# Kernel optimization log

Measured on AMD Instinct MI355X. Metric: run time of the kernel, lower is better.

Reference implementation:

```python
import jax, jax.numpy as jnp
import numpy as np

H = 8      # n_heads
DK = 64    # d_k per head
EPS = 1e-5       # InstanceNorm1d eps
SLOPE = 0.01     # LeakyReLU negative slope


def setup_inputs() -> dict:
    key = jax.random.key(0)
    ks = jax.random.split(key, 6)
    B, C, L = 16, 256, 1024
    HD = H * DK  # 512
    return {
        "x": jax.random.normal(ks[0], (B, C, L), dtype=jnp.float32),
        "Wq": jax.random.normal(ks[1], (HD, C), dtype=jnp.float32) * 0.02,
        "Wk": jax.random.normal(ks[2], (HD, C), dtype=jnp.float32) * 0.02,
        "Wv": jax.random.normal(ks[3], (HD, C), dtype=jnp.float32) * 0.02,
        "Wo": jax.random.normal(ks[4], (C, HD), dtype=jnp.float32) * 0.02,
        "gamma": jax.random.normal(ks[5], (1,), dtype=jnp.float32),
    }


def reference(x, Wq, Wk, Wv, Wo, gamma):
    B, C, L = x.shape
    # conv1x1 projections (bias=False) == channel matmuls -> [B, H*DK, L]
    # then reshape/permute into heads: [B, H, L, DK]
    def proj(W):
        y = jnp.einsum('oc,bcl->bol', W, x)          # [B, H*DK, L]
        return y.reshape(B, H, DK, L).transpose(0, 1, 3, 2)  # [B, H, L, DK]

    q, k, v = proj(Wq), proj(Wk), proj(Wv)
    # softmax-free linear attention: (Q K^T / d_k) V
    logits = jnp.einsum('bhld,bhmd->bhlm', q, k) / DK  # [B, H, L, L]
    out = jnp.einsum('bhlm,bhmd->bhld', logits, v)     # [B, H, L, DK]
    # merge heads back to channel-first [B, H*DK, L]
    merged = out.transpose(0, 1, 3, 2).reshape(B, H * DK, L)
    # output conv1x1 -> [B, C, L]
    o = jnp.einsum('oc,bcl->bol', Wo, merged)
    # InstanceNorm1d (affine=False): normalize over L per (b, c)
    mu = jnp.mean(o, axis=-1, keepdims=True)
    var = jnp.var(o, axis=-1, keepdims=True)
    o = (o - mu) * jax.lax.rsqrt(var + EPS)
    # gamma-scaled residual + LeakyReLU
    y = o * gamma + x
    return jnp.where(y >= 0, y, SLOPE * y)
```

## Files before the change

kernel.cpp:

```cpp
#include <hip/hip_runtime.h>

typedef __bf16 bf16;
typedef bf16 bf16x8 __attribute__((ext_vector_type(8)));
typedef bf16 bf16x4 __attribute__((ext_vector_type(4)));
typedef float f32x4 __attribute__((ext_vector_type(4)));

#define EPS 1e-5f
#define SLOPE 0.01f

__device__ __forceinline__ void gld_lds16(const bf16* g, bf16* l) {
    __builtin_amdgcn_global_load_lds(
        (const __attribute__((address_space(1))) unsigned int*)g,
        (__attribute__((address_space(3))) unsigned int*)l, 16, 0, 0);
}

template<int LOG2T>
__device__ __forceinline__ void xcd_decode(int raw, int& b, int& t) {
    const int p = raw & 7, m = raw >> 3;
    b = ((m >> LOG2T) << 3) + p;
    t = m & ((1 << LOG2T) - 1);
}

__global__ __launch_bounds__(256) void prep_kernel(
    const float* __restrict__ x,
    const float* __restrict__ Wq, const float* __restrict__ Wk,
    const float* __restrict__ Wv, const float* __restrict__ Wo,
    bf16* __restrict__ xT, bf16* __restrict__ xB,
    bf16* __restrict__ WkB, bf16* __restrict__ WvB,
    bf16* __restrict__ WoB, bf16* __restrict__ WqT)
{
    __shared__ float tile[64][65];
    const int raw = blockIdx.x;
    int id;
    if (raw < 1024) {
        int b, t64; xcd_decode<6>(raw, b, t64);
        id = (b << 6) | t64;
    } else id = raw;
    const int t = threadIdx.x;
    if (id < 1024) {
        const int lt = id & 15, ct = (id >> 4) & 3, b = id >> 6;
        {
            const int cl = t >> 2;
            const int l4 = (t & 3) << 4;
            const float* src = x + (size_t)(b * 256 + ct * 64 + cl) * 1024 + lt * 64 + l4;
            float4 v0 = ((const float4*)src)[0];
            float4 v1 = ((const float4*)src)[1];
            float4 v2 = ((const float4*)src)[2];
            float4 v3 = ((const float4*)src)[3];
            bf16x8 r0, r1;
            r0[0]=(bf16)v0.x; r0[1]=(bf16)v0.y; r0[2]=(bf16)v0.z; r0[3]=(bf16)v0.w;
            r0[4]=(bf16)v1.x; r0[5]=(bf16)v1.y; r0[6]=(bf16)v1.z; r0[7]=(bf16)v1.w;
            r1[0]=(bf16)v2.x; r1[1]=(bf16)v2.y; r1[2]=(bf16)v2.z; r1[3]=(bf16)v2.w;
            r1[4]=(bf16)v3.x; r1[5]=(bf16)v3.y; r1[6]=(bf16)v3.z; r1[7]=(bf16)v3.w;
            bf16* xbd = xB + (size_t)(b * 256 + ct * 64 + cl) * 1024 + lt * 64 + l4;
            *(bf16x8*)xbd = r0;
            *(bf16x8*)(xbd + 8) = r1;
            float* tr = &tile[cl][l4];
            tr[0]=v0.x; tr[1]=v0.y; tr[2]=v0.z; tr[3]=v0.w;
            tr[4]=v1.x; tr[5]=v1.y; tr[6]=v1.z; tr[7]=v1.w;
            tr[8]=v2.x; tr[9]=v2.y; tr[10]=v2.z; tr[11]=v2.w;
            tr[12]=v3.x; tr[13]=v3.y; tr[14]=v3.z; tr[15]=v3.w;
        }
        __syncthreads();
        {
            const int lw = t >> 2;
            const int ec = (t & 3) << 4;
            bf16x8 o0, o1;
            #pragma unroll
            for (int ii = 0; ii < 8; ++ii) {
                o0[ii] = (bf16)tile[ec + ii][lw];
                o1[ii] = (bf16)tile[ec + 8 + ii][lw];
            }
            bf16* dst = xT + (size_t)(b * 1024 + lt * 64 + lw) * 256 + ct * 64 + ec;
            *(bf16x8*)dst = o0;
            *(bf16x8*)(dst + 8) = o1;
        }
    } else if (id < 1408) {
        const int i = (id - 1024) * 1024 + t * 4;
        const float* src; bf16* dst;
        if (i < 131072)      { src = Wk + i;            dst = WkB + i; }
        else if (i < 262144) { src = Wv + (i - 131072); dst = WvB + (i - 131072); }
        else                 { src = Wo + (i - 262144); dst = WoB + (i - 262144); }
        float4 v = *(const float4*)src;
        bf16x4 o;
        o[0]=(bf16)v.x; o[1]=(bf16)v.y; o[2]=(bf16)v.z; o[3]=(bf16)v.w;
        *(bf16x4*)dst = o;
    } else {
        const int id2 = id - 1408;
        const int h = id2 >> 2, ct = id2 & 3;
        {
            const int e  = t >> 2;
            const int c4 = (t & 3) << 4;
            const float* src = Wq + (size_t)(h * 64 + e) * 256 + ct * 64 + c4;
            float4 v0 = ((const float4*)src)[0];
            float4 v1 = ((const float4*)src)[1];
            float4 v2 = ((const float4*)src)[2];
            float4 v3 = ((const float4*)src)[3];
            float* tr = &tile[e][c4];
            tr[0]=v0.x; tr[1]=v0.y; tr[2]=v0.z; tr[3]=v0.w;
            tr[4]=v1.x; tr[5]=v1.y; tr[6]=v1.z; tr[7]=v1.w;
            tr[8]=v2.x; tr[9]=v2.y; tr[10]=v2.z; tr[11]=v2.w;
            tr[12]=v3.x; tr[13]=v3.y; tr[14]=v3.z; tr[15]=v3.w;
        }
        __syncthreads();
        {
            const int c  = t >> 2;
            const int e4 = (t & 3) << 4;
            bf16x8 o0, o1;
            #pragma unroll
            for (int ii = 0; ii < 8; ++ii) {
                o0[ii] = (bf16)tile[e4 + ii][c];
                o1[ii] = (bf16)tile[e4 + 8 + ii][c];
            }
            bf16* dst = WqT + (size_t)h * 16384 + (size_t)(ct * 64 + c) * 64 + e4;
            *(bf16x8*)dst = o0;
            *(bf16x8*)(dst + 8) = o1;
        }
    }
}

template<int KDIM, typename OutT>
__global__ __launch_bounds__(256) void gemm128_bt(
    const bf16* __restrict__ A, const bf16* __restrict__ Bt, OutT* __restrict__ C,
    long long sA, long long sBt, long long sC, int ldC)
{
    constexpr int NT = KDIM / 32;
    constexpr int NB = 5;
    __shared__ bf16 As[NB][128 * 32];
    __shared__ bf16 Bs[NB][128 * 32];
    int z, tt; xcd_decode<4>(blockIdx.x, z, tt);
    A  += (size_t)z * sA;
    Bt += (size_t)z * sBt;
    C  += (size_t)z * sC;
    const int m0 = (tt >> 3) * 128;
    const int n0 = (tt & 7) * 128;
    const int t = threadIdx.x, w = t >> 6, l = t & 63;
    const int srow = w * 16 + (l >> 2);
    const int ske  = (l & 3) * 8;
    const bf16* ga = A  + (size_t)(m0 + srow) * KDIM + ske;
    const bf16* gb = Bt + (size_t)(n0 + srow) * KDIM + ske;
    const int loff = srow * 32 + ske;
    const int lm = l & 15, lq = l >> 4;
    const int wm = (w & 1) * 64, wn = (w >> 1) * 64;

    #pragma unroll
    for (int i = 0; i < NB - 1; ++i) {
        const int k0 = i * 32;
        gld_lds16(ga + k0, &As[i][0] + loff);
        gld_lds16(ga + k0 + (size_t)64 * KDIM, &As[i][0] + 64 * 32 + loff);
        gld_lds16(gb + k0, &Bs[i][0] + loff);
        gld_lds16(gb + k0 + (size_t)64 * KDIM, &Bs[i][0] + 64 * 32 + loff);
    }

    f32x4 acc[4][4] = {};
    #pragma unroll
    for (int kt = 0; kt < NT; ++kt) {
        const int cur = kt % NB;
        const int stg = (kt + NB - 1) % NB;
        const int remain = NT - 1 - kt;
        if (remain >= 3)      asm volatile("s_waitcnt vmcnt(12)" ::: "memory");
        else if (remain == 2) asm volatile("s_waitcnt vmcnt(8)"  ::: "memory");
        else if (remain == 1) asm volatile("s_waitcnt vmcnt(4)"  ::: "memory");
        else                  asm volatile("s_waitcnt vmcnt(0)"  ::: "memory");
        __builtin_amdgcn_s_barrier();
        __builtin_amdgcn_sched_barrier(0);
        if (kt + NB - 1 < NT) {
            const int k0 = (kt + NB - 1) * 32;
            gld_lds16(ga + k0, &As[stg][0] + loff);
            gld_lds16(ga + k0 + (size_t)64 * KDIM, &As[stg][0] + 64 * 32 + loff);
            gld_lds16(gb + k0, &Bs[stg][0] + loff);
            gld_lds16(gb + k0 + (size_t)64 * KDIM, &Bs[stg][0] + 64 * 32 + loff);
        }
        bf16x8 af[4], bfr[4];
        #pragma unroll
        for (int i = 0; i < 4; ++i)
            af[i] = *(const bf16x8*)(&As[cur][0] + (wm + i * 16 + lm) * 32 + lq * 8);
        #pragma unroll
        for (int j = 0; j < 4; ++j)
            bfr[j] = *(const bf16x8*)(&Bs[cur][0] + (wn + j * 16 + lm) * 32 + lq * 8);
        #pragma unroll
        for (int i = 0; i < 4; ++i)
            #pragma unroll
            for (int j = 0; j < 4; ++j)
                acc[i][j] = __builtin_amdgcn_mfma_f32_16x16x32_bf16(af[i], bfr[j], acc[i][j], 0, 0, 0);
    }
    #pragma unroll
    for (int i = 0; i < 4; ++i)
        #pragma unroll
        for (int j = 0; j < 4; ++j) {
            const int row = m0 + wm + i * 16 + lq * 4;
            const int col = n0 + wn + j * 16 + lm;
            OutT* cp = C + (size_t)row * ldC + col;
            #pragma unroll
            for (int r = 0; r < 4; ++r)
                cp[(size_t)r * ldC] = (OutT)acc[i][j][r];
        }
}

template<int KDIM, typename OutT>
__global__ __launch_bounds__(256) void gemm64_bt(
    const bf16* __restrict__ A, const bf16* __restrict__ Bt, OutT* __restrict__ C,
    long long sA, long long sBt, long long sC, int ldC)
{
    constexpr int NT = KDIM / 32;
    constexpr int NB = 5;
    __shared__ bf16 As[NB][64 * 32];
    __shared__ bf16 Bs[NB][64 * 32];
    int z, tt; xcd_decode<4>(blockIdx.x, z, tt);
    A  += (size_t)z * sA;
    Bt += (size_t)z * sBt;
    C  += (size_t)z * sC;
    const int m0 = (tt & 3) * 64;
    const int n0 = (tt >> 2) * 64;
    const int t = threadIdx.x, w = t >> 6, l = t & 63;
    const int srow = t >> 2;
    const int ske  = (t & 3) * 8;
    const bf16* ga = A  + (size_t)(m0 + srow) * KDIM + ske;
    const bf16* gb = Bt + (size_t)(n0 + srow) * KDIM + ske;
    const int loff = srow * 32 + ske;
    const int lm = l & 15, lq = l >> 4;

    #pragma unroll
    for (int i = 0; i < NB - 1; ++i) {
        const int k0 = i * 32;
        gld_lds16(ga + k0, &As[i][0] + loff);
        gld_lds16(gb + k0, &Bs[i][0] + loff);
    }

    f32x4 acc[4] = {};
    #pragma unroll
    for (int kt = 0; kt < NT; ++kt) {
        const int cur = kt % NB;
        const int stg = (kt + NB - 1) % NB;
        const int remain = NT - 1 - kt;
        if (remain >= 3)      asm volatile("s_waitcnt vmcnt(6)" ::: "memory");
        else if (remain == 2) asm volatile("s_waitcnt vmcnt(4)" ::: "memory");
        else if (remain == 1) asm volatile("s_waitcnt vmcnt(2)" ::: "memory");
        else                  asm volatile("s_waitcnt vmcnt(0)" ::: "memory");
        __builtin_amdgcn_s_barrier();
        __builtin_amdgcn_sched_barrier(0);
        if (kt + NB - 1 < NT) {
            const int k0 = (kt + NB - 1) * 32;
            gld_lds16(ga + k0, &As[stg][0] + loff);
            gld_lds16(gb + k0, &Bs[stg][0] + loff);
        }
        bf16x8 af = *(const bf16x8*)(&As[cur][0] + (w * 16 + lm) * 32 + lq * 8);
        bf16x8 bfr[4];
        #pragma unroll
        for (int j = 0; j < 4; ++j)
            bfr[j] = *(const bf16x8*)(&Bs[cur][0] + (j * 16 + lm) * 32 + lq * 8);
        #pragma unroll
        for (int j = 0; j < 4; ++j)
            acc[j] = __builtin_amdgcn_mfma_f32_16x16x32_bf16(af, bfr[j], acc[j], 0, 0, 0);
    }
    #pragma unroll
    for (int j = 0; j < 4; ++j) {
        const int row = m0 + w * 16 + lq * 4;
        const int col = n0 + j * 16 + lm;
        OutT* cp = C + (size_t)row * ldC + col;
        #pragma unroll
        for (int r = 0; r < 4; ++r)
            cp[(size_t)r * ldC] = (OutT)acc[j][r];
    }
}

struct __align__(16) Tm2Ph1 { bf16 P[16384]; bf16 Va[16384]; bf16 Gr[4][8192]; };
struct __align__(16) Tm2Ph2 { bf16 P[16384]; bf16 Kc[16384]; bf16 Qb[16384]; bf16 Tb[4096]; };
union  __align__(16) Tm2Sm  { Tm2Ph1 p1; Tm2Ph2 p2; };

__global__ __launch_bounds__(256) void tm2_kernel(
    const bf16* __restrict__ G, const bf16* __restrict__ WvB,
    const bf16* __restrict__ WkB, const bf16* __restrict__ WqT,
    bf16* __restrict__ WmT)
{
    __shared__ Tm2Sm sm;
    int b, h; xcd_decode<3>(blockIdx.x, b, h);
    const bf16* Gg = G   + (size_t)b * 65536;
    const bf16* Vg = WvB + (size_t)h * 16384;
    const bf16* Kg = WkB + (size_t)h * 16384;
    const bf16* Qg = WqT + (size_t)h * 16384;
    const int t = threadIdx.x, w = t >> 6, l = t & 63;
    const int lm = l & 15, lq = l >> 4;

    #pragma unroll
    for (int it = 0; it < 4; ++it) {
        const int idx = it * 256 + t;
        const int r = idx >> 2, s2 = idx & 3;
        gld_lds16(Gg + (size_t)r * 256 + 0 * 32 + (s2 ^ (r & 3)) * 8,
                  &sm.p1.Gr[0][0] + r * 32 + s2 * 8);
    }
    #pragma unroll
    for (int it = 0; it < 8; ++it) {
        const int idx = it * 256 + t;
        const int r = idx >> 5, s = idx & 31;
        gld_lds16(Vg + (size_t)r * 256 + (s ^ (r & 7)) * 8,
                  sm.p1.Va + r * 256 + s * 8);
    }
    #pragma unroll
    for (int tb = 1; tb < 3; ++tb) {
        #pragma unroll
        for (int it = 0; it < 4; ++it) {
            const int idx = it * 256 + t;
            const int r = idx >> 2, s2 = idx & 3;
            gld_lds16(Gg + (size_t)r * 256 + tb * 32 + (s2 ^ (r & 3)) * 8,
                      &sm.p1.Gr[tb][0] + r * 32 + s2 * 8);
        }
    }

    f32x4 accP[4][4] = {};
    #pragma unroll
    for (int kt = 0; kt < 8; ++kt) {
        if (kt <= 5)      asm volatile("s_waitcnt vmcnt(8)" ::: "memory");
        else if (kt == 6) asm volatile("s_waitcnt vmcnt(4)" ::: "memory");
        else              asm volatile("s_waitcnt vmcnt(0)" ::: "memory");
        __builtin_amdgcn_s_barrier();
        __builtin_amdgcn_sched_barrier(0);
        if (kt < 5) {
            const int tb = kt + 3;
            #pragma unroll
            for (int it = 0; it < 4; ++it) {
                const int idx = it * 256 + t;
                const int r = idx >> 2, s2 = idx & 3;
                gld_lds16(Gg + (size_t)r * 256 + tb * 32 + (s2 ^ (r & 3)) * 8,
                          &sm.p1.Gr[tb & 3][0] + r * 32 + s2 * 8);
            }
        }
        bf16x8 af[4], bfr[4];
        #pragma unroll
        for (int mf = 0; mf < 4; ++mf) {
            const int ra = mf * 16 + lm;
            af[mf] = *(const bf16x8*)(sm.p1.Va + ra * 256 + ((kt * 4 + lq) ^ (ra & 7)) * 8);
        }
        #pragma unroll
        for (int nf = 0; nf < 4; ++nf) {
            const int rb = w * 64 + nf * 16 + lm;
            bfr[nf] = *(const bf16x8*)(&sm.p1.Gr[kt & 3][0] + rb * 32 + (lq ^ (rb & 3)) * 8);
        }
        #pragma unroll
        for (int mf = 0; mf < 4; ++mf)
            #pragma unroll
            for (int nf = 0; nf < 4; ++nf)
                accP[mf][nf] = __builtin_amdgcn_mfma_f32_16x16x32_bf16(af[mf], bfr[nf], accP[mf][nf], 0, 0, 0);
    }
    #pragma unroll
    for (int mf = 0; mf < 4; ++mf)
        #pragma unroll
        for (int nf = 0; nf < 4; ++nf)
            #pragma unroll
            for (int ri = 0; ri < 4; ++ri) {
                const int d = mf * 16 + lq * 4 + ri;
                const int c = w * 64 + nf * 16 + lm;
                sm.p1.P[d * 256 + (((c >> 3) ^ (d & 7)) << 3) + (c & 7)] =
                    (bf16)accP[mf][nf][ri];
            }
    __syncthreads();

    #pragma unroll
    for (int it = 0; it < 8; ++it) {
        const int idx = it * 256 + t;
        const int r = idx >> 5, s = idx & 31;
        gld_lds16(Kg + (size_t)r * 256 + (s ^ (r & 7)) * 8,
                  sm.p2.Kc + r * 256 + s * 8);
    }
    #pragma unroll
    for (int it = 0; it < 8; ++it) {
        const int idx = it * 256 + t;
        const int r = idx >> 3, s2 = idx & 7;
        gld_lds16(Qg + (size_t)r * 64 + (s2 ^ (r & 7)) * 8,
                  sm.p2.Qb + r * 64 + s2 * 8);
    }

    asm volatile("s_waitcnt vmcnt(8)" ::: "memory");
    __builtin_amdgcn_s_barrier();
    __builtin_amdgcn_sched_barrier(0);
    f32x4 accT[4] = {};
    #pragma unroll
    for (int kk = 0; kk < 8; ++kk) {
        const int ra = w * 16 + lm;
        bf16x8 a = *(const bf16x8*)(sm.p2.P + ra * 256 + ((kk * 4 + lq) ^ (ra & 7)) * 8);
        #pragma unroll
        for (int nf = 0; nf < 4; ++nf) {
            const int rb = nf * 16 + lm;
            bf16x8 bb = *(const bf16x8*)(sm.p2.Kc + rb * 256 + ((kk * 4 + lq) ^ (rb & 7)) * 8);
            accT[nf] = __builtin_amdgcn_mfma_f32_16x16x32_bf16(a, bb, accT[nf], 0, 0, 0);
        }
    }
    #pragma unroll
    for (int nf = 0; nf < 4; ++nf)
        #pragma unroll
        for (int ri = 0; ri < 4; ++ri) {
            const int row = w * 16 + lq * 4 + ri;
            const int col = nf * 16 + lm;
            sm.p2.Tb[row * 64 + (((col >> 3) ^ (row & 7)) << 3) + (col & 7)] =
                (bf16)(accT[nf][ri] * 0.015625f);
        }
    asm volatile("s_waitcnt vmcnt(0)" ::: "memory");
    __syncthreads();

    f32x4 accM[4][4] = {};
    #pragma unroll
    for (int ks = 0; ks < 2; ++ks) {
        const int q = ks * 4 + lq;
        bf16x8 bfrag[4];
        #pragma unroll
        for (int nf = 0; nf < 4; ++nf) {
            const int rb = nf * 16 + lm;
            bfrag[nf] = *(const bf16x8*)(sm.p2.Tb + rb * 64 + (q ^ (rb & 7)) * 8);
        }
        #pragma unroll
        for (int mf = 0; mf < 4; ++mf) {
            const int ra = w * 64 + mf * 16 + lm;
            bf16x8 a = *(const bf16x8*)(sm.p2.Qb + ra * 64 + (q ^ (ra & 7)) * 8);
            #pragma unroll
            for (int nf = 0; nf < 4; ++nf)
                accM[mf][nf] = __builtin_amdgcn_mfma_f32_16x16x32_bf16(a, bfrag[nf], accM[mf][nf], 0, 0, 0);
        }
    }
    bf16* Wg = WmT + (size_t)b * 131072 + h * 64;
    #pragma unroll
    for (int mf = 0; mf < 4; ++mf)
        #pragma unroll
        for (int nf = 0; nf < 4; ++nf)
            #pragma unroll
            for (int ri = 0; ri < 4; ++ri) {
                const int c = w * 64 + mf * 16 + lq * 4 + ri;
                const int d = nf * 16 + lm;
                Wg[(size_t)c * 512 + d] = (bf16)accM[mf][nf][ri];
            }
}

__global__ __launch_bounds__(256) void norm_kernel(
    const bf16* __restrict__ o, const bf16* __restrict__ xB,
    const float* __restrict__ gamma, float* __restrict__ y)
{
    int b, c; xcd_decode<8>(blockIdx.x, b, c);
    const size_t row = ((size_t)b << 8) | c;
    const bf16* orow = o + row * 1024;
    const bf16* xrow = xB + row * 1024;
    float* yrow = y + row * 1024;
    const int tid = threadIdx.x;

    bf16x4 ov = *(const bf16x4*)(orow + tid * 4);
    float4 v = {(float)ov[0], (float)ov[1], (float)ov[2], (float)ov[3]};
    float s  = v.x + v.y + v.z + v.w;
    float ss = v.x * v.x + v.y * v.y + v.z * v.z + v.w * v.w;
    #pragma unroll
    for (int off = 32; off > 0; off >>= 1) {
        s  += __shfl_down(s, off);
        ss += __shfl_down(ss, off);
    }
    __shared__ float red[10];
    const int wave = tid >> 6, lane = tid & 63;
    if (lane == 0) { red[wave] = s; red[4 + wave] = ss; }
    __syncthreads();
    if (tid == 0) {
        float a  = red[0] + red[1] + red[2] + red[3];
        float b2 = red[4] + red[5] + red[6] + red[7];
        float mu = a * (1.0f / 1024.0f);
        float var = b2 * (1.0f / 1024.0f) - mu * mu;
        red[8] = mu;
        red[9] = rsqrtf(var + EPS);
    }
    __syncthreads();
    const float mu = red[8], inv = red[9], g = gamma[0];
    bf16x4 xv4 = *(const bf16x4*)(xrow + tid * 4);
    float4 r;
    r.x = (v.x - mu) * inv * g + (float)xv4[0];
    r.y = (v.y - mu) * inv * g + (float)xv4[1];
    r.z = (v.z - mu) * inv * g + (float)xv4[2];
    r.w = (v.w - mu) * inv * g + (float)xv4[3];
    r.x = r.x >= 0.f ? r.x : SLOPE * r.x;
    r.y = r.y >= 0.f ? r.y : SLOPE * r.y;
    r.z = r.z >= 0.f ? r.z : SLOPE * r.z;
    r.w = r.w >= 0.f ? r.w : SLOPE * r.w;
    ((float4*)yrow)[tid] = r;
}

extern "C" void kernel_launch(void* const* d_in, const int* in_sizes, int n_in,
                              void* d_out, int out_size, void* d_ws, size_t ws_size,
                              hipStream_t stream) {
    const float* x     = (const float*)d_in[0];
    const float* Wq    = (const float*)d_in[1];
    const float* Wk    = (const float*)d_in[2];
    const float* Wv    = (const float*)d_in[3];
    const float* Wo    = (const float*)d_in[4];
    const float* gamma = (const float*)d_in[5];
    float* y = (float*)d_out;

    char* wsb = (char*)d_ws;
    bf16* xT  = (bf16*)(wsb);
    bf16* xB  = (bf16*)(wsb +  8388608);
    bf16* WkB = (bf16*)(wsb + 16777216);
    bf16* WvB = (bf16*)(wsb + 17039360);
    bf16* WoB = (bf16*)(wsb + 17301504);
    bf16* WqT = (bf16*)(wsb + 17563648);
    bf16* G   = (bf16*)(wsb + 17825792);
    bf16* WmT = (bf16*)(wsb + 24117248);
    bf16* Wt  = (bf16*)(wsb + 28311552);
    bf16* o   = (bf16*)(wsb + 30408704);

    prep_kernel<<<dim3(1440), 256, 0, stream>>>(x, Wq, Wk, Wv, Wo, xT, xB, WkB, WvB, WoB, WqT);

    gemm64_bt<1024, bf16><<<dim3(256), 256, 0, stream>>>(
        xB, xB, G, 262144LL, 262144LL, 65536LL, 256);

    tm2_kernel<<<dim3(128), 256, 0, stream>>>(G, WvB, WkB, WqT, WmT);

    gemm64_bt<512, bf16><<<dim3(256), 256, 0, stream>>>(
        WoB, WmT, Wt, 0LL, 131072LL, 65536LL, 256);

    gemm128_bt<256, bf16><<<dim3(256), 256, 0, stream>>>(
        Wt, xT, o, 65536LL, 262144LL, 262144LL, 1024);

    norm_kernel<<<dim3(4096), 256, 0, stream>>>(o, xB, gamma, y);
}
```

Baseline: 120.7 us.

## Split tm2 work over head halves and process two rows per norm block

The tm2 kernel now splits each (batch, head) task into two halves over the value dimension. This doubles the grid from 128 to 256 blocks so more CUs are busy, at the cost of recomputing the K-side product share and loading K/Q in both halves. The norm kernel now handles two rows per block with 128 threads each, using 8-wide bf16 loads and removing the second barrier and single-thread reduction. Launch sizes are adjusted to match.

```diff
diff --git a/kernel.cpp b/kernel.cpp
--- a/kernel.cpp
+++ b/kernel.cpp
@@ -264,8 +264,8 @@
     }
 }
 
-struct __align__(16) Tm2Ph1 { bf16 P[16384]; bf16 Va[16384]; bf16 Gr[4][8192]; };
-struct __align__(16) Tm2Ph2 { bf16 P[16384]; bf16 Kc[16384]; bf16 Qb[16384]; bf16 Tb[4096]; };
+struct __align__(16) Tm2Ph1 { bf16 P[8192]; bf16 Va[8192]; bf16 Gr[4][8192]; };
+struct __align__(16) Tm2Ph2 { bf16 P[8192]; bf16 Kc[16384]; bf16 Qb[16384]; bf16 Tb[2048]; };
 union  __align__(16) Tm2Sm  { Tm2Ph1 p1; Tm2Ph2 p2; };
 
 __global__ __launch_bounds__(256) void tm2_kernel(
@@ -274,9 +274,10 @@
     bf16* __restrict__ WmT)
 {
     __shared__ Tm2Sm sm;
-    int b, h; xcd_decode<3>(blockIdx.x, b, h);
+    int b, tt; xcd_decode<4>(blockIdx.x, b, tt);
+    const int h = tt >> 1, half = tt & 1;
     const bf16* Gg = G   + (size_t)b * 65536;
-    const bf16* Vg = WvB + (size_t)h * 16384;
+    const bf16* Vg = WvB + (size_t)h * 16384 + half * 32 * 256;
     const bf16* Kg = WkB + (size_t)h * 16384;
     const bf16* Qg = WqT + (size_t)h * 16384;
     const int t = threadIdx.x, w = t >> 6, l = t & 63;
@@ -290,7 +291,7 @@
                   &sm.p1.Gr[0][0] + r * 32 + s2 * 8);
     }
     #pragma unroll
-    for (int it = 0; it < 8; ++it) {
+    for (int it = 0; it < 4; ++it) {
         const int idx = it * 256 + t;
         const int r = idx >> 5, s = idx & 31;
         gld_lds16(Vg + (size_t)r * 256 + (s ^ (r & 7)) * 8,
@@ -307,7 +308,7 @@
         }
     }
 
-    f32x4 accP[4][4] = {};
+    f32x4 accP[2][4] = {};
     #pragma unroll
     for (int kt = 0; kt < 8; ++kt) {
         if (kt <= 5)      asm volatile("s_waitcnt vmcnt(8)" ::: "memory");
@@ -325,9 +326,9 @@
                           &sm.p1.Gr[tb & 3][0] + r * 32 + s2 * 8);
             }
         }
-        bf16x8 af[4], bfr[4];
-        #pragma unroll
-        for (int mf = 0; mf < 4; ++mf) {
+        bf16x8 af[2], bfr[4];
+        #pragma unroll
+        for (int mf = 0; mf < 2; ++mf) {
             const int ra = mf * 16 + lm;
             af[mf] = *(const bf16x8*)(sm.p1.Va + ra * 256 + ((kt * 4 + lq) ^ (ra & 7)) * 8);
         }
@@ -337,13 +338,13 @@
             bfr[nf] = *(const bf16x8*)(&sm.p1.Gr[kt & 3][0] + rb * 32 + (lq ^ (rb & 3)) * 8);
         }
         #pragma unroll
-        for (int mf = 0; mf < 4; ++mf)
+        for (int mf = 0; mf < 2; ++mf)
             #pragma unroll
             for (int nf = 0; nf < 4; ++nf)
                 accP[mf][nf] = __builtin_amdgcn_mfma_f32_16x16x32_bf16(af[mf], bfr[nf], accP[mf][nf], 0, 0, 0);
     }
     #pragma unroll
-    for (int mf = 0; mf < 4; ++mf)
+    for (int mf = 0; mf < 2; ++mf)
         #pragma unroll
         for (int nf = 0; nf < 4; ++nf)
             #pragma unroll
@@ -373,37 +374,37 @@
     asm volatile("s_waitcnt vmcnt(8)" ::: "memory");
     __builtin_amdgcn_s_barrier();
     __builtin_amdgcn_sched_barrier(0);
-    f32x4 accT[4] = {};
+    f32x4 accT[2] = {};
     #pragma unroll
     for (int kk = 0; kk < 8; ++kk) {
-        const int ra = w * 16 + lm;
-        bf16x8 a = *(const bf16x8*)(sm.p2.P + ra * 256 + ((kk * 4 + lq) ^ (ra & 7)) * 8);
-        #pragma unroll
-        for (int nf = 0; nf < 4; ++nf) {
-            const int rb = nf * 16 + lm;
-            bf16x8 bb = *(const bf16x8*)(sm.p2.Kc + rb * 256 + ((kk * 4 + lq) ^ (rb & 7)) * 8);
-            accT[nf] = __builtin_amdgcn_mfma_f32_16x16x32_bf16(a, bb, accT[nf], 0, 0, 0);
-        }
-    }
-    #pragma unroll
-    for (int nf = 0; nf < 4; ++nf)
+        const int rb = w * 16 + lm;
+        bf16x8 bb = *(const bf16x8*)(sm.p2.Kc + rb * 256 + ((kk * 4 + lq) ^ (rb & 7)) * 8);
+        #pragma unroll
+        for (int mf = 0; mf < 2; ++mf) {
+            const int ra = mf * 16 + lm;
+            bf16x8 a = *(const bf16x8*)(sm.p2.P + ra * 256 + ((kk * 4 + lq) ^ (ra & 7)) * 8);
+            accT[mf] = __builtin_amdgcn_mfma_f32_16x16x32_bf16(a, bb, accT[mf], 0, 0, 0);
+        }
+    }
+    #pragma unroll
+    for (int mf = 0; mf < 2; ++mf)
         #pragma unroll
         for (int ri = 0; ri < 4; ++ri) {
-            const int row = w * 16 + lq * 4 + ri;
-            const int col = nf * 16 + lm;
+            const int row = mf * 16 + lq * 4 + ri;
+            const int col = w * 16 + lm;
             sm.p2.Tb[row * 64 + (((col >> 3) ^ (row & 7)) << 3) + (col & 7)] =
-                (bf16)(accT[nf][ri] * 0.015625f);
+                (bf16)(accT[mf][ri] * 0.015625f);
         }
     asm volatile("s_waitcnt vmcnt(0)" ::: "memory");
     __syncthreads();
 
-    f32x4 accM[4][4] = {};
+    f32x4 accM[4][2] = {};
     #pragma unroll
     for (int ks = 0; ks < 2; ++ks) {
         const int q = ks * 4 + lq;
-        bf16x8 bfrag[4];
-        #pragma unroll
-        for (int nf = 0; nf < 4; ++nf) {
+        bf16x8 bfrag[2];
+        #pragma unroll
+        for (int nf = 0; nf < 2; ++nf) {
             const int rb = nf * 16 + lm;
             bfrag[nf] = *(const bf16x8*)(sm.p2.Tb + rb * 64 + (q ^ (rb & 7)) * 8);
         }
@@ -412,15 +413,15 @@
             const int ra = w * 64 + mf * 16 + lm;
             bf16x8 a = *(const bf16x8*)(sm.p2.Qb + ra * 64 + (q ^ (ra & 7)) * 8);
             #pragma unroll
-            for (int nf = 0; nf < 4; ++nf)
+            for (int nf = 0; nf < 2; ++nf)
                 accM[mf][nf] = __builtin_amdgcn_mfma_f32_16x16x32_bf16(a, bfrag[nf], accM[mf][nf], 0, 0, 0);
         }
     }
-    bf16* Wg = WmT + (size_t)b * 131072 + h * 64;
+    bf16* Wg = WmT + (size_t)b * 131072 + h * 64 + half * 32;
     #pragma unroll
     for (int mf = 0; mf < 4; ++mf)
         #pragma unroll
-        for (int nf = 0; nf < 4; ++nf)
+        for (int nf = 0; nf < 2; ++nf)
             #pragma unroll
             for (int ri = 0; ri < 4; ++ri) {
                 const int c = w * 64 + mf * 16 + lq * 4 + ri;
@@ -433,47 +434,50 @@
     const bf16* __restrict__ o, const bf16* __restrict__ xB,
     const float* __restrict__ gamma, float* __restrict__ y)
 {
-    int b, c; xcd_decode<8>(blockIdx.x, b, c);
-    const size_t row = ((size_t)b << 8) | c;
+    int b, rp; xcd_decode<7>(blockIdx.x, b, rp);
+    const int tid = threadIdx.x;
+    const int w2 = tid >> 7;
+    const int ti = tid & 127;
+    const size_t row = ((size_t)b << 8) | (rp * 2 + w2);
     const bf16* orow = o + row * 1024;
     const bf16* xrow = xB + row * 1024;
     float* yrow = y + row * 1024;
-    const int tid = threadIdx.x;
-
-    bf16x4 ov = *(const bf16x4*)(orow + tid * 4);
-    float4 v = {(float)ov[0], (float)ov[1], (float)ov[2], (float)ov[3]};
-    float s  = v.x + v.y + v.z + v.w;
-    float ss = v.x * v.x + v.y * v.y + v.z * v.z + v.w * v.w;
+
+    bf16x8 ov = *(const bf16x8*)(orow + ti * 8);
+    float v[8];
+    float s = 0.f, ss = 0.f;
+    #pragma unroll
+    for (int i = 0; i < 8; ++i) {
+        v[i] = (float)ov[i];
+        s += v[i]; ss += v[i] * v[i];
+    }
     #pragma unroll
     for (int off = 32; off > 0; off >>= 1) {
         s  += __shfl_down(s, off);
         ss += __shfl_down(ss, off);
     }
-    __shared__ float red[10];
+    __shared__ float red[8];
     const int wave = tid >> 6, lane = tid & 63;
     if (lane == 0) { red[wave] = s; red[4 + wave] = ss; }
     __syncthreads();
-    if (tid == 0) {
-        float a  = red[0] + red[1] + red[2] + red[3];
-        float b2 = red[4] + red[5] + red[6] + red[7];
-        float mu = a * (1.0f / 1024.0f);
-        float var = b2 * (1.0f / 1024.0f) - mu * mu;
-        red[8] = mu;
-        red[9] = rsqrtf(var + EPS);
-    }
-    __syncthreads();
-    const float mu = red[8], inv = red[9], g = gamma[0];
-    bf16x4 xv4 = *(const bf16x4*)(xrow + tid * 4);
-    float4 r;
-    r.x = (v.x - mu) * inv * g + (float)xv4[0];
-    r.y = (v.y - mu) * inv * g + (float)xv4[1];
-    r.z = (v.z - mu) * inv * g + (float)xv4[2];
-    r.w = (v.w - mu) * inv * g + (float)xv4[3];
-    r.x = r.x >= 0.f ? r.x : SLOPE * r.x;
-    r.y = r.y >= 0.f ? r.y : SLOPE * r.y;
-    r.z = r.z >= 0.f ? r.z : SLOPE * r.z;
-    r.w = r.w >= 0.f ? r.w : SLOPE * r.w;
-    ((float4*)yrow)[tid] = r;
+    const float a  = red[w2 * 2] + red[w2 * 2 + 1];
+    const float b2 = red[4 + w2 * 2] + red[4 + w2 * 2 + 1];
+    const float mu = a * (1.0f / 1024.0f);
+    const float var = b2 * (1.0f / 1024.0f) - mu * mu;
+    const float inv = rsqrtf(var + EPS);
+    const float g = gamma[0];
+
+    bf16x8 xv = *(const bf16x8*)(xrow + ti * 8);
+    float r[8];
+    #pragma unroll
+    for (int i = 0; i < 8; ++i) {
+        float rr = (v[i] - mu) * inv * g + (float)xv[i];
+        r[i] = rr >= 0.f ? rr : SLOPE * rr;
+    }
+    float4 r0 = {r[0], r[1], r[2], r[3]};
+    float4 r1 = {r[4], r[5], r[6], r[7]};
+    ((float4*)(yrow + ti * 8))[0] = r0;
+    ((float4*)(yrow + ti * 8 + 4))[0] = r1;
 }
 
 extern "C" void kernel_launch(void* const* d_in, const int* in_sizes, int n_in,
@@ -504,7 +508,7 @@
     gemm64_bt<1024, bf16><<<dim3(256), 256, 0, stream>>>(
         xB, xB, G, 262144LL, 262144LL, 65536LL, 256);
 
-    tm2_kernel<<<dim3(128), 256, 0, stream>>>(G, WvB, WkB, WqT, WmT);
+    tm2_kernel<<<dim3(256), 256, 0, stream>>>(G, WvB, WkB, WqT, WmT);
 
     gemm64_bt<512, bf16><<<dim3(256), 256, 0, stream>>>(
         WoB, WmT, Wt, 0LL, 131072LL, 65536LL, 256);
@@ -512,5 +516,5 @@
     gemm128_bt<256, bf16><<<dim3(256), 256, 0, stream>>>(
         Wt, xT, o, 65536LL, 262144LL, 262144LL, 1024);
 
-    norm_kernel<<<dim3(4096), 256, 0, stream>>>(o, xB, gamma, y);
-}
+    norm_kernel<<<dim3(2048), 256, 0, stream>>>(o, xB, gamma, y);
+}
```

Result: no change. 119.3 us (-1.1%).
